# Performance work log

Measured on AMD Instinct MI355X. Metric: run time of the kernel, lower is better.

Reference implementation:

```python
import jax, jax.numpy as jnp
import numpy as np

MARGIN = 0.2
SCALE = 30.0
EPS_NORM = 1e-12
EPS_COS = 1e-7

B, D, C = 4096, 256, 5994


def setup_inputs() -> dict:
    key = jax.random.key(0)
    kx, kw, kl = jax.random.split(key, 3)
    x = jax.random.normal(kx, (B, D), dtype=jnp.float32)
    # xavier_normal_ init: std = sqrt(2 / (fan_in + fan_out))
    w_std = np.sqrt(2.0 / (D + C)).astype(np.float32)
    W = jax.random.normal(kw, (D, C), dtype=jnp.float32) * w_std
    label = jax.random.randint(kl, (B,), 0, C, dtype=jnp.int64)
    return {"x": x, "W": W, "label": label}


def reference(x, W, label):
    # L2-normalize rows of x and columns of W
    xn = x / jnp.clip(jnp.linalg.norm(x, axis=1, keepdims=True), EPS_NORM)
    wn = W / jnp.clip(jnp.linalg.norm(W, axis=0, keepdims=True), EPS_NORM)
    # cosine similarity logits [B, C]
    costh = xn @ wn
    # faithful clamp (note: original clamps upper bound to 1+eps)
    costh = jnp.clip(costh, -1.0 + EPS_COS, 1.0 + EPS_COS)
    theta = jnp.arccos(costh)
    costh_m = jnp.cos(theta + MARGIN)
    # apply margin only on the target class, then scale
    one_hot = jnp.arange(costh.shape[1])[None, :] == label[:, None]  # [B, C] bool
    output = jnp.where(one_hot, costh_m, costh) * SCALE
    # cross entropy (mean over batch)
    logp = jax.nn.log_softmax(output, axis=-1)
    loss = -jnp.mean(jnp.take_along_axis(logp, label[:, None], axis=1))
    # top-1 accuracy in percent
    acc = jnp.mean((jnp.argmax(output, axis=-1) == label).astype(jnp.float32)) * 100.0
    return loss, acc
```

## Files before the change

### kernel.cpp

```cpp
#include <hip/hip_runtime.h>
#include <hip/hip_bf16.h>
#include <hip/hip_fp8.h>

#define BB 4096
#define DD 256
#define CC 5994
#define CPAD 6144
#define PARTS 32
#define NCH 12
#define COSM 0.9800665778412416f
#define SINM 0.19866933079506122f

typedef __attribute__((ext_vector_type(4))) float f32x4;

__device__ __forceinline__ unsigned char f2fp8(float f) {
  return __hip_fp8_e4m3(f).__x;
}

__global__ void k_prep(const float* __restrict__ x, const float* __restrict__ W,
                       unsigned char* __restrict__ xnS, unsigned char* __restrict__ wnS,
                       unsigned* __restrict__ accum) {
  int b = blockIdx.x;
  int t = threadIdx.x;
  if (b < 1024) {
    int tgi = t >> 6, l = t & 63;
    int row = b * 4 + tgi;
    float4 v = reinterpret_cast<const float4*>(x + (size_t)row * DD)[l];
    float ss = v.x * v.x + v.y * v.y + v.z * v.z + v.w * v.w;
#pragma unroll
    for (int m = 32; m >= 1; m >>= 1) ss += __shfl_xor(ss, m, 64);
    float inv = 1.0f / fmaxf(sqrtf(ss), 1e-12f);
    unsigned wd = (unsigned)f2fp8(v.x * inv) |
                  ((unsigned)f2fp8(v.y * inv) << 8) |
                  ((unsigned)f2fp8(v.z * inv) << 16) |
                  ((unsigned)f2fp8(v.w * inv) << 24);
    int off = (row >> 4) * 4096 + (l >> 3) * 512 + ((l >> 1) & 3) * 128 + (row & 15) * 8 + (l & 1) * 4;
    *reinterpret_cast<unsigned*>(xnS + off) = wd;
  } else {
    if (b == 1024 && t < 4) accum[t] = 0u;
    __shared__ float pp[16][17];
    __shared__ float sinv[16];
    int lr = t & 15, u = t >> 4;
    int bb = b - 1024;
    int chunk = (bb & 7) * 48 + (bb >> 3);
    int c = chunk * 16 + lr;
    int D0 = u * 16;
    float v[16];
    float ss = 0.f;
#pragma unroll
    for (int i = 0; i < 16; ++i) {
      float xv = (c < CC) ? W[(size_t)(D0 + i) * CC + c] : 0.f;
      v[i] = xv; ss += xv * xv;
    }
    pp[u][lr] = ss;
    __syncthreads();
    if (t < 16) {
      float tot = 0.f;
#pragma unroll
      for (int g = 0; g < 16; ++g) tot += pp[g][t];
      sinv[t] = (chunk * 16 + t < CC) ? 1.0f / fmaxf(sqrtf(tot), 1e-12f) : 0.f;
    }
    __syncthreads();
    float inv = sinv[lr];
    int base = chunk * 4096 + (u >> 1) * 512 + ((2 * u) & 3) * 128 + lr * 8;
    unsigned long long w0 = 0ull, w1 = 0ull;
#pragma unroll
    for (int i = 0; i < 8; ++i)
      w0 |= ((unsigned long long)f2fp8(v[i] * inv)) << (8 * i);
#pragma unroll
    for (int i = 0; i < 8; ++i)
      w1 |= ((unsigned long long)f2fp8(v[8 + i] * inv)) << (8 * i);
    *reinterpret_cast<unsigned long long*>(wnS + base) = w0;
    *reinterpret_cast<unsigned long long*>(wnS + base + 128) = w1;
  }
}

__launch_bounds__(256, 2)
__global__ void k_main(const unsigned char* __restrict__ xnS,
                       const unsigned char* __restrict__ wnS,
                       const int* __restrict__ label,
                       float* __restrict__ sp, float* __restrict__ vmp,
                       float* __restrict__ vtp) {
  int bid = blockIdx.x;
  int sw = (bid & 7) * 128 + (bid >> 3);
  int part = sw >> 5;
  int rowblk = sw & 31;
  int t = threadIdx.x, w = t >> 6, l = t & 63;
  int lg = l >> 4, lr = l & 15;
  int r0 = rowblk * 128 + w * 32;

  long a[2][8];
#pragma unroll
  for (int rt = 0; rt < 2; ++rt) {
    const unsigned char* ap = xnS + ((r0 >> 4) + rt) * 4096 + lg * 128 + lr * 8;
#pragma unroll
    for (int ks = 0; ks < 8; ++ks)
      a[rt][ks] = *reinterpret_cast<const long*>(ap + ks * 512);
  }
  int lab[8];
#pragma unroll
  for (int rt = 0; rt < 2; ++rt)
#pragma unroll
    for (int j = 0; j < 4; ++j) lab[rt * 4 + j] = label[r0 + rt * 16 + lg * 4 + j];

  float s[8], vm[8], vt[8];
#pragma unroll
  for (int i = 0; i < 8; ++i) { s[i] = 0.f; vm[i] = -2.f; vt[i] = -2.f; }

  const unsigned char* bbase = wnS + (size_t)part * 49152 + l * 8;
  long b[8];
#pragma unroll
  for (int ks = 0; ks < 8; ++ks)
    b[ks] = *reinterpret_cast<const long*>(bbase + ks * 512);

#pragma unroll 2
  for (int c = 0; c < NCH; ++c) {
    long bn[8];
    if (c + 1 < NCH) {
      const unsigned char* bp = bbase + (c + 1) * 4096;
#pragma unroll
      for (int ks = 0; ks < 8; ++ks)
        bn[ks] = *reinterpret_cast<const long*>(bp + ks * 512);
    }
    f32x4 acc0 = {0.f, 0.f, 0.f, 0.f}, acc1 = {0.f, 0.f, 0.f, 0.f};
#pragma unroll
    for (int ks = 0; ks < 8; ++ks) {
      acc0 = __builtin_amdgcn_mfma_f32_16x16x32_fp8_fp8(a[0][ks], b[ks], acc0, 0, 0, 0);
      acc1 = __builtin_amdgcn_mfma_f32_16x16x32_fp8_fp8(a[1][ks], b[ks], acc1, 0, 0, 0);
    }
    int col = part * 192 + c * 16 + lr;
#pragma unroll
    for (int j = 0; j < 4; ++j) {
      float v0 = acc0[j], v1 = acc1[j];
      s[j]     += __expf(__builtin_fmaf(v0, 30.f, -30.f));
      s[4 + j] += __expf(__builtin_fmaf(v1, 30.f, -30.f));
      bool i0 = (col == lab[j]), i1 = (col == lab[4 + j]);
      vt[j]     = i0 ? v0 : vt[j];
      vt[4 + j] = i1 ? v1 : vt[4 + j];
      vm[j]     = fmaxf(vm[j],     i0 ? -2.f : v0);
      vm[4 + j] = fmaxf(vm[4 + j], i1 ? -2.f : v1);
    }
#pragma unroll
    for (int ks = 0; ks < 8; ++ks) b[ks] = bn[ks];
  }

#pragma unroll
  for (int i = 0; i < 8; ++i) {
#pragma unroll
    for (int mk = 1; mk < 16; mk <<= 1) {
      s[i] += __shfl_xor(s[i], mk, 64);
      vm[i] = fmaxf(vm[i], __shfl_xor(vm[i], mk, 64));
      vt[i] = fmaxf(vt[i], __shfl_xor(vt[i], mk, 64));
    }
    if (lr == 0) {
      int row = r0 + (i >> 2) * 16 + lg * 4 + (i & 3);
      int idx = row * PARTS + part;
      sp[idx] = s[i]; vmp[idx] = vm[i]; vtp[idx] = vt[i];
    }
  }
}

__global__ void k_tail(const float* __restrict__ sp, const float* __restrict__ vmp,
                       const float* __restrict__ vtp, float* __restrict__ accum,
                       float* __restrict__ out) {
  int t = threadIdx.x;
  int row = blockIdx.x * 64 + t;
  float s = 0.f, vm = -2.f, vt = -2.f;
#pragma unroll
  for (int q = 0; q < 8; ++q) {
    float4 aq = reinterpret_cast<const float4*>(sp + row * PARTS)[q];
    float4 mq = reinterpret_cast<const float4*>(vmp + row * PARTS)[q];
    float4 tq = reinterpret_cast<const float4*>(vtp + row * PARTS)[q];
    s += aq.x + aq.y + aq.z + aq.w;
    vm = fmaxf(vm, fmaxf(fmaxf(mq.x, mq.y), fmaxf(mq.z, mq.w)));
    vt = fmaxf(vt, fmaxf(fmaxf(tq.x, tq.y), fmaxf(tq.z, tq.w)));
  }
  float vtc = fminf(fmaxf(vt, -1.f + 1e-7f), 1.f + 1e-7f);
  float sn = sqrtf(fmaxf(1.f - vtc * vtc, 0.f));
  float tg = 30.f * (vtc * COSM - sn * SINM);
  float sadj = s - __expf(30.f * vt - 30.f) + __expf(tg - 30.f);
  float loss = 30.f + logf(sadj) - tg;
  float corr = (tg >= 30.f * vm) ? 1.f : 0.f;
#pragma unroll
  for (int mk = 32; mk >= 1; mk >>= 1) {
    loss += __shfl_xor(loss, mk, 64);
    corr += __shfl_xor(corr, mk, 64);
  }
  if (t == 0) {
    atomicAdd(accum + 0, loss);
    atomicAdd(accum + 1, corr);
    __threadfence();
    unsigned ticket = atomicAdd(reinterpret_cast<unsigned*>(accum) + 2, 1u);
    if (ticket == 63) {
      float L = atomicAdd(accum + 0, 0.0f);
      float Cr = atomicAdd(accum + 1, 0.0f);
      out[0] = L / (float)BB;
      out[1] = Cr * (100.0f / (float)BB);
    }
  }
}

extern "C" void kernel_launch(void* const* d_in, const int* in_sizes, int n_in,
                              void* d_out, int out_size, void* d_ws, size_t ws_size,
                              hipStream_t stream) {
  const float* x = (const float*)d_in[0];
  const float* W = (const float*)d_in[1];
  const int* label = (const int*)d_in[2];
  float* out = (float*)d_out;

  char* ws = (char*)d_ws;
  unsigned char* wnS = (unsigned char*)(ws);
  unsigned char* xnS = (unsigned char*)(ws + 1572864);
  size_t po = 2621440;
  float* sp  = (float*)(ws + po);
  float* vmp = (float*)(ws + po + 524288);
  float* vtp = (float*)(ws + po + 1048576);
  float* accum = (float*)(ws + po + 1572864);

  k_prep<<<1408, 256, 0, stream>>>(x, W, xnS, wnS, (unsigned*)accum);
  k_main<<<1024, 256, 0, stream>>>(xnS, wnS, label, sp, vmp, vtp);
  k_tail<<<BB / 64, 64, 0, stream>>>(sp, vmp, vtp, accum, out);
}
```

Before: 35.11 us.

## Repack fp8 operands so each lane loads contiguous 64 bytes with 128-bit loads

Changes the swizzled fp8 layout of normalized x and W so each lane's eight K-slices sit contiguously in 64 bytes. The main kernel then reads them with four 16-byte vector loads instead of eight 8-byte strided loads. The manual double-buffered prefetch is replaced by a fully unrolled chunk loop, leaving load scheduling to the compiler. Fewer, wider memory instructions are the aim, but the unrolled loop may raise register pressure, and the new access pattern spreads each wave's loads over 4 KB.

After: 42.34 us. +20.6%, slower.

```diff
diff --git a/kernel.cpp b/kernel.cpp
--- a/kernel.cpp
+++ b/kernel.cpp
@@ -12,6 +12,7 @@
 #define SINM 0.19866933079506122f
 
 typedef __attribute__((ext_vector_type(4))) float f32x4;
+typedef __attribute__((ext_vector_type(2))) long longx2;
 
 __device__ __forceinline__ unsigned char f2fp8(float f) {
   return __hip_fp8_e4m3(f).__x;
@@ -34,7 +35,7 @@
                   ((unsigned)f2fp8(v.y * inv) << 8) |
                   ((unsigned)f2fp8(v.z * inv) << 16) |
                   ((unsigned)f2fp8(v.w * inv) << 24);
-    int off = (row >> 4) * 4096 + (l >> 3) * 512 + ((l >> 1) & 3) * 128 + (row & 15) * 8 + (l & 1) * 4;
+    int off = (row >> 4) * 4096 + (((l >> 1) & 3) * 16 + (row & 15)) * 64 + (l >> 3) * 8 + (l & 1) * 4;
     *reinterpret_cast<unsigned*>(xnS + off) = wd;
   } else {
     if (b == 1024 && t < 4) accum[t] = 0u;
@@ -62,7 +63,6 @@
     }
     __syncthreads();
     float inv = sinv[lr];
-    int base = chunk * 4096 + (u >> 1) * 512 + ((2 * u) & 3) * 128 + lr * 8;
     unsigned long long w0 = 0ull, w1 = 0ull;
 #pragma unroll
     for (int i = 0; i < 8; ++i)
@@ -70,8 +70,11 @@
 #pragma unroll
     for (int i = 0; i < 8; ++i)
       w1 |= ((unsigned long long)f2fp8(v[8 + i] * inv)) << (8 * i);
-    *reinterpret_cast<unsigned long long*>(wnS + base) = w0;
-    *reinterpret_cast<unsigned long long*>(wnS + base + 128) = w1;
+    int lgb = (u & 1) * 2;
+    int base0 = chunk * 4096 + (lgb * 16 + lr) * 64 + (u >> 1) * 8;
+    int base1 = chunk * 4096 + ((lgb + 1) * 16 + lr) * 64 + (u >> 1) * 8;
+    *reinterpret_cast<unsigned long long*>(wnS + base0) = w0;
+    *reinterpret_cast<unsigned long long*>(wnS + base1) = w1;
   }
 }
 
@@ -92,10 +95,12 @@
   long a[2][8];
 #pragma unroll
   for (int rt = 0; rt < 2; ++rt) {
-    const unsigned char* ap = xnS + ((r0 >> 4) + rt) * 4096 + lg * 128 + lr * 8;
-#pragma unroll
-    for (int ks = 0; ks < 8; ++ks)
-      a[rt][ks] = *reinterpret_cast<const long*>(ap + ks * 512);
+    const longx2* ap = reinterpret_cast<const longx2*>(xnS + ((r0 >> 4) + rt) * 4096 + l * 64);
+#pragma unroll
+    for (int i = 0; i < 4; ++i) {
+      longx2 q = ap[i];
+      a[rt][2 * i] = q.x; a[rt][2 * i + 1] = q.y;
+    }
   }
   int lab[8];
 #pragma unroll
@@ -107,27 +112,29 @@
 #pragma unroll
   for (int i = 0; i < 8; ++i) { s[i] = 0.f; vm[i] = -2.f; vt[i] = -2.f; }
 
-  const unsigned char* bbase = wnS + (size_t)part * 49152 + l * 8;
-  long b[8];
-#pragma unroll
-  for (int ks = 0; ks < 8; ++ks)
-    b[ks] = *reinterpret_cast<const long*>(bbase + ks * 512);
-
-#pragma unroll 2
+  const unsigned char* bbase = wnS + (size_t)part * 49152 + l * 64;
+
+#pragma unroll
   for (int c = 0; c < NCH; ++c) {
-    long bn[8];
-    if (c + 1 < NCH) {
-      const unsigned char* bp = bbase + (c + 1) * 4096;
-#pragma unroll
-      for (int ks = 0; ks < 8; ++ks)
-        bn[ks] = *reinterpret_cast<const long*>(bp + ks * 512);
-    }
+    const longx2* bp = reinterpret_cast<const longx2*>(bbase + c * 4096);
+    longx2 q0 = bp[0], q1 = bp[1], q2 = bp[2], q3 = bp[3];
     f32x4 acc0 = {0.f, 0.f, 0.f, 0.f}, acc1 = {0.f, 0.f, 0.f, 0.f};
-#pragma unroll
-    for (int ks = 0; ks < 8; ++ks) {
-      acc0 = __builtin_amdgcn_mfma_f32_16x16x32_fp8_fp8(a[0][ks], b[ks], acc0, 0, 0, 0);
-      acc1 = __builtin_amdgcn_mfma_f32_16x16x32_fp8_fp8(a[1][ks], b[ks], acc1, 0, 0, 0);
-    }
+    acc0 = __builtin_amdgcn_mfma_f32_16x16x32_fp8_fp8(a[0][0], q0.x, acc0, 0, 0, 0);
+    acc1 = __builtin_amdgcn_mfma_f32_16x16x32_fp8_fp8(a[1][0], q0.x, acc1, 0, 0, 0);
+    acc0 = __builtin_amdgcn_mfma_f32_16x16x32_fp8_fp8(a[0][1], q0.y, acc0, 0, 0, 0);
+    acc1 = __builtin_amdgcn_mfma_f32_16x16x32_fp8_fp8(a[1][1], q0.y, acc1, 0, 0, 0);
+    acc0 = __builtin_amdgcn_mfma_f32_16x16x32_fp8_fp8(a[0][2], q1.x, acc0, 0, 0, 0);
+    acc1 = __builtin_amdgcn_mfma_f32_16x16x32_fp8_fp8(a[1][2], q1.x, acc1, 0, 0, 0);
+    acc0 = __builtin_amdgcn_mfma_f32_16x16x32_fp8_fp8(a[0][3], q1.y, acc0, 0, 0, 0);
+    acc1 = __builtin_amdgcn_mfma_f32_16x16x32_fp8_fp8(a[1][3], q1.y, acc1, 0, 0, 0);
+    acc0 = __builtin_amdgcn_mfma_f32_16x16x32_fp8_fp8(a[0][4], q2.x, acc0, 0, 0, 0);
+    acc1 = __builtin_amdgcn_mfma_f32_16x16x32_fp8_fp8(a[1][4], q2.x, acc1, 0, 0, 0);
+    acc0 = __builtin_amdgcn_mfma_f32_16x16x32_fp8_fp8(a[0][5], q2.y, acc0, 0, 0, 0);
+    acc1 = __builtin_amdgcn_mfma_f32_16x16x32_fp8_fp8(a[1][5], q2.y, acc1, 0, 0, 0);
+    acc0 = __builtin_amdgcn_mfma_f32_16x16x32_fp8_fp8(a[0][6], q3.x, acc0, 0, 0, 0);
+    acc1 = __builtin_amdgcn_mfma_f32_16x16x32_fp8_fp8(a[1][6], q3.x, acc1, 0, 0, 0);
+    acc0 = __builtin_amdgcn_mfma_f32_16x16x32_fp8_fp8(a[0][7], q3.y, acc0, 0, 0, 0);
+    acc1 = __builtin_amdgcn_mfma_f32_16x16x32_fp8_fp8(a[1][7], q3.y, acc1, 0, 0, 0);
     int col = part * 192 + c * 16 + lr;
 #pragma unroll
     for (int j = 0; j < 4; ++j) {
@@ -140,8 +147,6 @@
       vm[j]     = fmaxf(vm[j],     i0 ? -2.f : v0);
       vm[4 + j] = fmaxf(vm[4 + j], i1 ? -2.f : v1);
     }
-#pragma unroll
-    for (int ks = 0; ks < 8; ++ks) b[ks] = bn[ks];
   }
 
 #pragma unroll
```
